# Optimization experiments

Measured on AMD Instinct MI355X. Metric: run time of the kernel, lower is better.

The kernel has to match this reference:

```python
import jax, jax.numpy as jnp
import numpy as np

L, E, D = 4, 512, 256   # layers, model dim (=2*D bidirectional), per-direction hidden
T, B = 100, 1000
EPS = 1e-5

def _layernorm(x, g, b):
    m = x.mean(-1, keepdims=True)
    v = x.var(-1, keepdims=True)
    return (x - m) / jnp.sqrt(v + EPS) * g + b

def _dir_scan(U, vf, vr, bf, br):
    # U: (T, B, 4, D) pre-projected gates; SRU elementwise recurrence over time.
    def step(c, u):
        f = jax.nn.sigmoid(u[:, 1] + vf * c + bf)
        c2 = f * c + (1.0 - f) * u[:, 0]
        r = jax.nn.sigmoid(u[:, 2] + vr * c2 + br)
        h = r * c2 + (1.0 - r) * u[:, 3]   # highway with projected residual u3
        return c2, h
    c0 = jnp.zeros((U.shape[1], U.shape[-1]), U.dtype)
    _, H = jax.lax.scan(step, c0, U)
    return H

def setup_inputs() -> dict:
    key = jax.random.key(0)
    ks = jax.random.split(key, 6)
    return {
        "sentence": jax.random.normal(ks[0], (T, B, E), jnp.float32),
        "sru_W": jax.random.normal(ks[1], (L, 2, E, 4 * D), jnp.float32) / np.float32(np.sqrt(E)),
        "sru_v": jax.random.normal(ks[2], (L, 2, 2, D), jnp.float32) * 0.05,
        "sru_b": jnp.zeros((L, 2, 2, D), jnp.float32),
        "ln_g": jnp.ones((L, E), jnp.float32),
        "ln_b": jnp.zeros((L, E), jnp.float32),
        "W1": jax.random.normal(ks[3], (E, E), jnp.float32) / np.float32(np.sqrt(E)),
        "b1": jnp.zeros((E,), jnp.float32),
        "bn_g": jnp.ones((E,), jnp.float32),
        "bn_b": jnp.zeros((E,), jnp.float32),
        "bn_mean": jnp.zeros((E,), jnp.float32),
        "bn_var": jnp.ones((E,), jnp.float32),
        "W2": jax.random.normal(ks[4], (E, 4), jnp.float32) / np.float32(np.sqrt(E)),
        "b2": jnp.zeros((4,), jnp.float32),
    }

def reference(sentence, sru_W, sru_v, sru_b, ln_g, ln_b, W1, b1, bn_g, bn_b, bn_mean, bn_var, W2, b2):
    x = sentence  # (T, B, E)
    for l in range(L):
        xl = _layernorm(x, ln_g[l], ln_b[l])
        # batched projection for both directions: (2, T, B, 4, D)
        U = jnp.einsum('tbi,dik->dtbk', xl, sru_W[l]).reshape(2, T, B, 4, D)
        Hf = _dir_scan(U[0], sru_v[l, 0, 0], sru_v[l, 0, 1], sru_b[l, 0, 0], sru_b[l, 0, 1])
        Hb = _dir_scan(U[1][::-1], sru_v[l, 1, 0], sru_v[l, 1, 1], sru_b[l, 1, 0], sru_b[l, 1, 1])[::-1]
        x = jnp.concatenate([Hf, Hb], axis=-1)  # (T, B, E)
    # head on flattened tokens (eval mode: dropout off, BN uses running stats)
    h = x.reshape(-1, E) @ W1 + b1
    h = (h - bn_mean) / jnp.sqrt(bn_var + EPS) * bn_g + bn_b
    h = jax.nn.relu(h)
    logits = h @ W2 + b2  # (T*B, 4)
    return jax.nn.log_softmax(logits, axis=-1)
```

## Files before the change

kernel.cpp:

```cpp
#include <hip/hip_runtime.h>
#include <stdint.h>

#define T_DIM 100
#define B_DIM 1000
#define E_DIM 512
#define D_DIM 256
#define L_DIM 4
#define M_TOK (T_DIM * B_DIM)
#define M_PAD 100096
#define K_DIM 512

typedef unsigned short u16;
typedef __bf16 bf16x8 __attribute__((ext_vector_type(8)));
typedef float f32x4 __attribute__((ext_vector_type(4)));
typedef unsigned short ushort8 __attribute__((ext_vector_type(8)));

__device__ __forceinline__ u16 f2bf(float f) {
  unsigned int u = __builtin_bit_cast(unsigned int, f);
  u += 0x7fffu + ((u >> 16) & 1u);
  return (u16)(u >> 16);
}
__device__ __forceinline__ float bf2f(u16 h) {
  unsigned int u = ((unsigned int)h) << 16;
  return __builtin_bit_cast(float, u);
}

__device__ __forceinline__ void gld16(const u16* g, u16* l) {
  __builtin_amdgcn_global_load_lds(
      (const __attribute__((address_space(1))) unsigned int*)g,
      (__attribute__((address_space(3))) unsigned int*)l, 16, 0, 0);
}

__global__ void transpose_cast(const float* __restrict__ in, u16* __restrict__ out,
                               int R, int C) {
  __shared__ float t[32][33];
  const int s = blockIdx.z;
  const float* ib = in + (size_t)s * R * C;
  u16* ob = out + (size_t)s * R * C;
  const int c0 = blockIdx.x * 32, r0 = blockIdx.y * 32;
  const int tx = threadIdx.x, ty = threadIdx.y;
#pragma unroll
  for (int j = 0; j < 4; ++j)
    t[ty + j * 8][tx] = ib[(size_t)(r0 + ty + j * 8) * C + c0 + tx];
  __syncthreads();
#pragma unroll
  for (int j = 0; j < 4; ++j)
    ob[(size_t)(c0 + ty + j * 8) * R + r0 + tx] = f2bf(t[tx][ty + j * 8]);
}

__global__ __launch_bounds__(256) void zero_pad(u16* __restrict__ xl) {
  const int i = blockIdx.x * 256 + threadIdx.x;
  ushort8 z = {0, 0, 0, 0, 0, 0, 0, 0};
  *(ushort8*)(xl + (size_t)M_TOK * 512 + (size_t)i * 8) = z;
}

template <typename TI>
__global__ __launch_bounds__(256) void ln_cast_kernel(
    const TI* __restrict__ x, const float* __restrict__ g,
    const float* __restrict__ b, u16* __restrict__ out) {
  const int wid = threadIdx.x >> 6, lane = threadIdx.x & 63;
  const int row = blockIdx.x * 4 + wid;
  float xe[8];
  if constexpr (sizeof(TI) == 4) {
    const float* xr = (const float*)x + (size_t)row * E_DIM + lane * 8;
    const float4 a = *(const float4*)xr;
    const float4 c = *(const float4*)(xr + 4);
    xe[0] = a.x; xe[1] = a.y; xe[2] = a.z; xe[3] = a.w;
    xe[4] = c.x; xe[5] = c.y; xe[6] = c.z; xe[7] = c.w;
  } else {
    const u16* xr = (const u16*)x + (size_t)row * E_DIM + lane * 8;
    const ushort8 hv = *(const ushort8*)xr;
#pragma unroll
    for (int u = 0; u < 8; ++u) xe[u] = bf2f(hv[u]);
  }
  float s = 0.f, q = 0.f;
#pragma unroll
  for (int u = 0; u < 8; ++u) { s += xe[u]; q += xe[u] * xe[u]; }
#pragma unroll
  for (int off = 32; off; off >>= 1) {
    s += __shfl_xor(s, off, 64);
    q += __shfl_xor(q, off, 64);
  }
  const float mean = s * (1.0f / 512.0f);
  const float var = q * (1.0f / 512.0f) - mean * mean;
  const float rstd = rsqrtf(var + 1e-5f);
  const float4 g0 = *(const float4*)(g + lane * 8);
  const float4 g1 = *(const float4*)(g + lane * 8 + 4);
  const float4 b0 = *(const float4*)(b + lane * 8);
  const float4 b1v = *(const float4*)(b + lane * 8 + 4);
  float ge[8] = {g0.x, g0.y, g0.z, g0.w, g1.x, g1.y, g1.z, g1.w};
  float be[8] = {b0.x, b0.y, b0.z, b0.w, b1v.x, b1v.y, b1v.z, b1v.w};
  ushort8 o;
#pragma unroll
  for (int u = 0; u < 8; ++u)
    o[u] = f2bf((xe[u] - mean) * rstd * ge[u] + be[u]);
  *(ushort8*)(out + (size_t)row * E_DIM + lane * 8) = o;
}

__global__ __launch_bounds__(256, 4) void gemm_bf16(
    const u16* __restrict__ A, const u16* __restrict__ B, u16* __restrict__ C,
    int N, int ntil_shift) {
  __shared__ u16 As[128 * 32];
  __shared__ u16 Bs[128 * 32];
  const int tid = threadIdx.x;
  const int wave = tid >> 6, lane = tid & 63;
  const int wm = wave >> 1, wn = wave & 1;
  const int nz = blockIdx.x;
  const int z = nz >> ntil_shift;
  const int n0 = (nz & ((1 << ntil_shift) - 1)) << 7;
  const size_t m0 = (size_t)blockIdx.y * 128;

  const int c_ld = (lane & 3) ^ ((lane >> 3) & 3);
  const u16* Ag = A + (m0 + wave * 32 + (lane >> 2)) * K_DIM + c_ld * 8;
  const u16* Bg = B + ((size_t)z * N + n0 + wave * 32 + (lane >> 2)) * K_DIM +
                  c_ld * 8;
  u16* Al = As + wave * 1024;
  u16* Bl = Bs + wave * 1024;

  f32x4 acc[4][4] = {};
  const int rA = lane & 15;
  const int ch = lane >> 4;
  const int sw = (ch ^ ((rA >> 1) & 3)) * 8;

  for (int kt = 0; kt < K_DIM; kt += 32) {
    gld16(Ag + kt, Al);
    gld16(Ag + kt + 16 * K_DIM, Al + 512);
    gld16(Bg + kt, Bl);
    gld16(Bg + kt + 16 * K_DIM, Bl + 512);
    __syncthreads();

    bf16x8 af[4], bfr[4];
#pragma unroll
    for (int mi = 0; mi < 4; ++mi)
      af[mi] = *(const bf16x8*)&As[(wm * 64 + mi * 16 + rA) * 32 + sw];
#pragma unroll
    for (int ni = 0; ni < 4; ++ni)
      bfr[ni] = *(const bf16x8*)&Bs[(wn * 64 + ni * 16 + rA) * 32 + sw];
#pragma unroll
    for (int mi = 0; mi < 4; ++mi)
#pragma unroll
      for (int ni = 0; ni < 4; ++ni)
        acc[mi][ni] = __builtin_amdgcn_mfma_f32_16x16x32_bf16(
            af[mi], bfr[ni], acc[mi][ni], 0, 0, 0);
    __syncthreads();
  }

  u16* Cb = C + (size_t)z * M_PAD * N;
  const int rr = (lane >> 4) * 4;
  const int cc = lane & 15;
#pragma unroll
  for (int mi = 0; mi < 4; ++mi) {
#pragma unroll
    for (int ni = 0; ni < 4; ++ni) {
      const size_t row = m0 + wm * 64 + mi * 16 + rr;
      const int col = n0 + wn * 64 + ni * 16 + cc;
#pragma unroll
      for (int r = 0; r < 4; ++r)
        Cb[(row + r) * N + col] = f2bf(acc[mi][ni][r]);
    }
  }
}

__global__ __launch_bounds__(256) void sru_scan(const u16* __restrict__ U,
                                                const float* __restrict__ v,
                                                const float* __restrict__ bb,
                                                u16* __restrict__ xout) {
  const int d = threadIdx.x;
  const int b = blockIdx.x;
  const int dir = blockIdx.y;
  const float vf = v[(dir * 2 + 0) * 256 + d];
  const float vr = v[(dir * 2 + 1) * 256 + d];
  const float bf = bb[(dir * 2 + 0) * 256 + d];
  const float br = bb[(dir * 2 + 1) * 256 + d];
  const u16* Ud = U + (size_t)dir * M_PAD * 1024;
  float c = 0.f;
  for (int s = 0; s < T_DIM; ++s) {
    const int t = dir ? (T_DIM - 1 - s) : s;
    const size_t base = ((size_t)t * B_DIM + b) * 1024 + d;
    const float u0 = bf2f(Ud[base]);
    const float u1 = bf2f(Ud[base + 256]);
    const float u2 = bf2f(Ud[base + 512]);
    const float u3 = bf2f(Ud[base + 768]);
    const float f = 1.f / (1.f + __expf(-(u1 + vf * c + bf)));
    c = f * c + (1.f - f) * u0;
    const float r = 1.f / (1.f + __expf(-(u2 + vr * c + br)));
    const float h = r * c + (1.f - r) * u3;
    xout[((size_t)t * B_DIM + b) * 512 + dir * 256 + d] = f2bf(h);
  }
}

__global__ __launch_bounds__(256) void head_kernel(
    const u16* __restrict__ h, const float* __restrict__ b1,
    const float* __restrict__ bn_g, const float* __restrict__ bn_b,
    const float* __restrict__ bn_mean, const float* __restrict__ bn_var,
    const float* __restrict__ W2, const float* __restrict__ b2,
    float* __restrict__ out) {
  const int wid = threadIdx.x >> 6, lane = threadIdx.x & 63;
  const int row = blockIdx.x * 4 + wid;
  const u16* hr = h + (size_t)row * E_DIM + lane * 8;
  const ushort8 hv = *(const ushort8*)hr;
  float s0 = 0.f, s1 = 0.f, s2 = 0.f, s3 = 0.f;
  const int j0 = lane * 8;
#pragma unroll
  for (int u = 0; u < 8; ++u) {
    const int j = j0 + u;
    const float hb = bf2f(hv[u]) + b1[j];
    float hn = (hb - bn_mean[j]) * rsqrtf(bn_var[j] + 1e-5f) * bn_g[j] + bn_b[j];
    hn = fmaxf(hn, 0.f);
    const float4 w = *(const float4*)(W2 + j * 4);
    s0 += hn * w.x; s1 += hn * w.y; s2 += hn * w.z; s3 += hn * w.w;
  }
#pragma unroll
  for (int off = 32; off; off >>= 1) {
    s0 += __shfl_xor(s0, off, 64);
    s1 += __shfl_xor(s1, off, 64);
    s2 += __shfl_xor(s2, off, 64);
    s3 += __shfl_xor(s3, off, 64);
  }
  if (lane == 0) {
    const float4 bv = *(const float4*)b2;
    const float l0 = s0 + bv.x, l1 = s1 + bv.y, l2 = s2 + bv.z, l3 = s3 + bv.w;
    const float mx = fmaxf(fmaxf(l0, l1), fmaxf(l2, l3));
    const float lse =
        mx + logf(__expf(l0 - mx) + __expf(l1 - mx) + __expf(l2 - mx) + __expf(l3 - mx));
    float4 o = {l0 - lse, l1 - lse, l2 - lse, l3 - lse};
    *(float4*)(out + (size_t)row * 4) = o;
  }
}

extern "C" void kernel_launch(void* const* d_in, const int* in_sizes, int n_in,
                              void* d_out, int out_size, void* d_ws, size_t ws_size,
                              hipStream_t stream) {
  const float* sentence = (const float*)d_in[0];
  const float* sru_W = (const float*)d_in[1];
  const float* sru_v = (const float*)d_in[2];
  const float* sru_b = (const float*)d_in[3];
  const float* ln_g = (const float*)d_in[4];
  const float* ln_b = (const float*)d_in[5];
  const float* W1 = (const float*)d_in[6];
  const float* b1 = (const float*)d_in[7];
  const float* bn_g = (const float*)d_in[8];
  const float* bn_b = (const float*)d_in[9];
  const float* bn_mean = (const float*)d_in[10];
  const float* bn_var = (const float*)d_in[11];
  const float* W2 = (const float*)d_in[12];
  const float* b2 = (const float*)d_in[13];

  char* ws = (char*)d_ws;
  const size_t XL_OFF = 0;
  const size_t X_OFF = XL_OFF + (size_t)M_PAD * 512 * 2;
  const size_t U_OFF = X_OFF + (size_t)M_TOK * 512 * 2;
  const size_t WT_OFF = U_OFF + (size_t)2 * M_PAD * 1024 * 2;
  const size_t W1T_OFF = WT_OFF + (size_t)8 * 512 * 1024 * 2;
  u16* xl = (u16*)(ws + XL_OFF);
  u16* x_buf = (u16*)(ws + X_OFF);
  u16* U = (u16*)(ws + U_OFF);
  u16* WT = (u16*)(ws + WT_OFF);
  u16* W1T = (u16*)(ws + W1T_OFF);
  u16* hbuf = U;

  transpose_cast<<<dim3(32, 16, 8), dim3(32, 8), 0, stream>>>(sru_W, WT, 512, 1024);
  transpose_cast<<<dim3(16, 16, 1), dim3(32, 8), 0, stream>>>(W1, W1T, 512, 512);
  zero_pad<<<24, 256, 0, stream>>>(xl);

  for (int l = 0; l < L_DIM; ++l) {
    if (l == 0)
      ln_cast_kernel<float><<<M_TOK / 4, 256, 0, stream>>>(
          sentence, ln_g, ln_b, xl);
    else
      ln_cast_kernel<u16><<<M_TOK / 4, 256, 0, stream>>>(
          x_buf, ln_g + l * 512, ln_b + l * 512, xl);
    gemm_bf16<<<dim3(16, M_PAD / 128), 256, 0, stream>>>(
        xl, WT + (size_t)l * 2 * 1024 * 512, U, 1024, 3);
    u16* xo = (l == L_DIM - 1) ? xl : x_buf;
    sru_scan<<<dim3(1000, 2), 256, 0, stream>>>(U, sru_v + l * 1024,
                                                sru_b + l * 1024, xo);
  }
  gemm_bf16<<<dim3(4, M_PAD / 128), 256, 0, stream>>>(xl, W1T, hbuf, 512, 2);
  head_kernel<<<M_TOK / 4, 256, 0, stream>>>(hbuf, b1, bn_g, bn_b, bn_mean,
                                             bn_var, W2, b2, (float*)d_out);
}
```

Baseline: 2.220 ms.

## Fuse SRU scan with next-layer LayerNorm, interleave gate columns, XCD-aware GEMM tiling

The weight transpose permutes output columns so the four SRU gates for each hidden unit sit next to each other. The scan can then fetch all four with one 8-byte load, prefetched two timesteps ahead. For layers 0-2, a new per-batch-element kernel runs both directions, keeps the full 100x512 hidden sequence in shared memory and applies the next layer's LayerNorm before writing. This removes the x_buf round trip and the separate LN launches. The GEMM grid is flattened with an XCD-aware block-to-tile mapping, and M is padded to a multiple of 1024. The catch is the ~100KB of LDS per scan block, which limits occupancy to one block per CU, and only 1000 blocks are available for the recurrence.

```diff
diff --git a/kernel.cpp b/kernel.cpp
--- a/kernel.cpp
+++ b/kernel.cpp
@@ -7,7 +7,7 @@
 #define D_DIM 256
 #define L_DIM 4
 #define M_TOK (T_DIM * B_DIM)
-#define M_PAD 100096
+#define M_PAD 100352
 #define K_DIM 512
 
 typedef unsigned short u16;
@@ -31,6 +31,7 @@
       (__attribute__((address_space(3))) unsigned int*)l, 16, 0, 0);
 }
 
+template <bool PERM>
 __global__ void transpose_cast(const float* __restrict__ in, u16* __restrict__ out,
                                int R, int C) {
   __shared__ float t[32][33];
@@ -44,8 +45,11 @@
     t[ty + j * 8][tx] = ib[(size_t)(r0 + ty + j * 8) * C + c0 + tx];
   __syncthreads();
 #pragma unroll
-  for (int j = 0; j < 4; ++j)
-    ob[(size_t)(c0 + ty + j * 8) * R + r0 + tx] = f2bf(t[tx][ty + j * 8]);
+  for (int j = 0; j < 4; ++j) {
+    const int c = c0 + ty + j * 8;
+    const int pc = PERM ? (((c & 255) << 2) | (c >> 8)) : c;
+    ob[(size_t)pc * R + r0 + tx] = f2bf(t[tx][ty + j * 8]);
+  }
 }
 
 __global__ __launch_bounds__(256) void zero_pad(u16* __restrict__ xl) {
@@ -54,25 +58,15 @@
   *(ushort8*)(xl + (size_t)M_TOK * 512 + (size_t)i * 8) = z;
 }
 
-template <typename TI>
 __global__ __launch_bounds__(256) void ln_cast_kernel(
-    const TI* __restrict__ x, const float* __restrict__ g,
+    const float* __restrict__ x, const float* __restrict__ g,
     const float* __restrict__ b, u16* __restrict__ out) {
   const int wid = threadIdx.x >> 6, lane = threadIdx.x & 63;
   const int row = blockIdx.x * 4 + wid;
-  float xe[8];
-  if constexpr (sizeof(TI) == 4) {
-    const float* xr = (const float*)x + (size_t)row * E_DIM + lane * 8;
-    const float4 a = *(const float4*)xr;
-    const float4 c = *(const float4*)(xr + 4);
-    xe[0] = a.x; xe[1] = a.y; xe[2] = a.z; xe[3] = a.w;
-    xe[4] = c.x; xe[5] = c.y; xe[6] = c.z; xe[7] = c.w;
-  } else {
-    const u16* xr = (const u16*)x + (size_t)row * E_DIM + lane * 8;
-    const ushort8 hv = *(const ushort8*)xr;
-#pragma unroll
-    for (int u = 0; u < 8; ++u) xe[u] = bf2f(hv[u]);
-  }
+  const float* xr = x + (size_t)row * E_DIM + lane * 8;
+  const float4 a = *(const float4*)xr;
+  const float4 c = *(const float4*)(xr + 4);
+  float xe[8] = {a.x, a.y, a.z, a.w, c.x, c.y, c.z, c.w};
   float s = 0.f, q = 0.f;
 #pragma unroll
   for (int u = 0; u < 8; ++u) { s += xe[u]; q += xe[u] * xe[u]; }
@@ -99,16 +93,23 @@
 
 __global__ __launch_bounds__(256, 4) void gemm_bf16(
     const u16* __restrict__ A, const u16* __restrict__ B, u16* __restrict__ C,
-    int N, int ntil_shift) {
+    int log2N, int ntil_shift) {
   __shared__ u16 As[128 * 32];
   __shared__ u16 Bs[128 * 32];
   const int tid = threadIdx.x;
   const int wave = tid >> 6, lane = tid & 63;
   const int wm = wave >> 1, wn = wave & 1;
-  const int nz = blockIdx.x;
-  const int z = nz >> ntil_shift;
-  const int n0 = (nz & ((1 << ntil_shift) - 1)) << 7;
-  const size_t m0 = (size_t)blockIdx.y * 128;
+
+  const int bid = blockIdx.x;
+  const int xcd = bid & 7;
+  const int j = bid >> 3;
+  const int nt = j & ((1 << ntil_shift) - 1);
+  const int mg = j >> ntil_shift;
+  const size_t m0 = (size_t)(xcd + (mg << 3)) * 128;
+  const int N = 1 << log2N;
+  const int colflat = nt << 7;
+  const int z = colflat >> log2N;
+  const int n0 = colflat & (N - 1);
 
   const int c_ld = (lane & 3) ^ ((lane >> 3) & 3);
   const u16* Ag = A + (m0 + wave * 32 + (lane >> 2)) * K_DIM + c_ld * 8;
@@ -158,6 +159,71 @@
       for (int r = 0; r < 4; ++r)
         Cb[(row + r) * N + col] = f2bf(acc[mi][ni][r]);
     }
+  }
+}
+
+__global__ __launch_bounds__(512) void sru_scan_ln(
+    const u16* __restrict__ U, const float* __restrict__ v,
+    const float* __restrict__ bb, const float* __restrict__ g,
+    const float* __restrict__ be, u16* __restrict__ xl) {
+  __shared__ u16 H[100 * 512];
+  const int b = blockIdx.x;
+  const int dir = threadIdx.x >> 8;
+  const int d = threadIdx.x & 255;
+  const float vf = v[(dir * 2 + 0) * 256 + d];
+  const float vr = v[(dir * 2 + 1) * 256 + d];
+  const float bfv = bb[(dir * 2 + 0) * 256 + d];
+  const float brv = bb[(dir * 2 + 1) * 256 + d];
+  const u16* p = U + (size_t)dir * M_PAD * 1024 +
+                 ((size_t)(dir ? (T_DIM - 1) : 0) * B_DIM + b) * 1024 + d * 4;
+  const intptr_t dstep = dir ? -(intptr_t)B_DIM * 1024 : (intptr_t)B_DIM * 1024;
+  ushort4 ua = *(const ushort4*)p;
+  ushort4 ub = *(const ushort4*)(p + dstep);
+  float c = 0.f;
+  int t = dir ? (T_DIM - 1) : 0;
+  const int tstep = dir ? -1 : 1;
+  for (int s = 0; s < T_DIM; ++s) {
+    ushort4 un = ub;
+    if (s + 2 < T_DIM) un = *(const ushort4*)(p + 2 * dstep);
+    const float u0 = bf2f(ua.x), u1 = bf2f(ua.y);
+    const float u2 = bf2f(ua.z), u3 = bf2f(ua.w);
+    const float f = 1.f / (1.f + __expf(-(u1 + vf * c + bfv)));
+    c = f * c + (1.f - f) * u0;
+    const float r = 1.f / (1.f + __expf(-(u2 + vr * c + brv)));
+    const float h = r * c + (1.f - r) * u3;
+    H[t * 512 + (dir << 8) + d] = f2bf(h);
+    ua = ub; ub = un; p += dstep; t += tstep;
+  }
+  __syncthreads();
+  const int wid = threadIdx.x >> 6, lane = threadIdx.x & 63;
+  const float4 g0 = *(const float4*)(g + lane * 8);
+  const float4 g1 = *(const float4*)(g + lane * 8 + 4);
+  const float4 b0 = *(const float4*)(be + lane * 8);
+  const float4 b1v = *(const float4*)(be + lane * 8 + 4);
+  const float ge[8] = {g0.x, g0.y, g0.z, g0.w, g1.x, g1.y, g1.z, g1.w};
+  const float bev[8] = {b0.x, b0.y, b0.z, b0.w, b1v.x, b1v.y, b1v.z, b1v.w};
+  for (int tr = wid; tr < T_DIM; tr += 8) {
+    const ushort8 hv = *(const ushort8*)&H[tr * 512 + lane * 8];
+    float xe[8];
+    float s = 0.f, q = 0.f;
+#pragma unroll
+    for (int u = 0; u < 8; ++u) {
+      xe[u] = bf2f(hv[u]);
+      s += xe[u]; q += xe[u] * xe[u];
+    }
+#pragma unroll
+    for (int off = 32; off; off >>= 1) {
+      s += __shfl_xor(s, off, 64);
+      q += __shfl_xor(q, off, 64);
+    }
+    const float mean = s * (1.0f / 512.0f);
+    const float var = q * (1.0f / 512.0f) - mean * mean;
+    const float rstd = rsqrtf(var + 1e-5f);
+    ushort8 o;
+#pragma unroll
+    for (int u = 0; u < 8; ++u)
+      o[u] = f2bf((xe[u] - mean) * rstd * ge[u] + bev[u]);
+    *(ushort8*)(xl + ((size_t)tr * B_DIM + b) * 512 + lane * 8) = o;
   }
 }
 
@@ -170,22 +236,27 @@
   const int dir = blockIdx.y;
   const float vf = v[(dir * 2 + 0) * 256 + d];
   const float vr = v[(dir * 2 + 1) * 256 + d];
-  const float bf = bb[(dir * 2 + 0) * 256 + d];
-  const float br = bb[(dir * 2 + 1) * 256 + d];
-  const u16* Ud = U + (size_t)dir * M_PAD * 1024;
+  const float bfv = bb[(dir * 2 + 0) * 256 + d];
+  const float brv = bb[(dir * 2 + 1) * 256 + d];
+  const u16* p = U + (size_t)dir * M_PAD * 1024 +
+                 ((size_t)(dir ? (T_DIM - 1) : 0) * B_DIM + b) * 1024 + d * 4;
+  const intptr_t dstep = dir ? -(intptr_t)B_DIM * 1024 : (intptr_t)B_DIM * 1024;
+  ushort4 ua = *(const ushort4*)p;
+  ushort4 ub = *(const ushort4*)(p + dstep);
   float c = 0.f;
+  int t = dir ? (T_DIM - 1) : 0;
+  const int tstep = dir ? -1 : 1;
   for (int s = 0; s < T_DIM; ++s) {
-    const int t = dir ? (T_DIM - 1 - s) : s;
-    const size_t base = ((size_t)t * B_DIM + b) * 1024 + d;
-    const float u0 = bf2f(Ud[base]);
-    const float u1 = bf2f(Ud[base + 256]);
-    const float u2 = bf2f(Ud[base + 512]);
-    const float u3 = bf2f(Ud[base + 768]);
-    const float f = 1.f / (1.f + __expf(-(u1 + vf * c + bf)));
+    ushort4 un = ub;
+    if (s + 2 < T_DIM) un = *(const ushort4*)(p + 2 * dstep);
+    const float u0 = bf2f(ua.x), u1 = bf2f(ua.y);
+    const float u2 = bf2f(ua.z), u3 = bf2f(ua.w);
+    const float f = 1.f / (1.f + __expf(-(u1 + vf * c + bfv)));
     c = f * c + (1.f - f) * u0;
-    const float r = 1.f / (1.f + __expf(-(u2 + vr * c + br)));
+    const float r = 1.f / (1.f + __expf(-(u2 + vr * c + brv)));
     const float h = r * c + (1.f - r) * u3;
-    xout[((size_t)t * B_DIM + b) * 512 + dir * 256 + d] = f2bf(h);
+    xout[((size_t)t * B_DIM + b) * 512 + (dir << 8) + d] = f2bf(h);
+    ua = ub; ub = un; p += dstep; t += tstep;
   }
 }
 
@@ -248,35 +319,33 @@
 
   char* ws = (char*)d_ws;
   const size_t XL_OFF = 0;
-  const size_t X_OFF = XL_OFF + (size_t)M_PAD * 512 * 2;
-  const size_t U_OFF = X_OFF + (size_t)M_TOK * 512 * 2;
+  const size_t U_OFF = XL_OFF + (size_t)M_PAD * 512 * 2;
   const size_t WT_OFF = U_OFF + (size_t)2 * M_PAD * 1024 * 2;
   const size_t W1T_OFF = WT_OFF + (size_t)8 * 512 * 1024 * 2;
   u16* xl = (u16*)(ws + XL_OFF);
-  u16* x_buf = (u16*)(ws + X_OFF);
   u16* U = (u16*)(ws + U_OFF);
   u16* WT = (u16*)(ws + WT_OFF);
   u16* W1T = (u16*)(ws + W1T_OFF);
   u16* hbuf = U;
 
-  transpose_cast<<<dim3(32, 16, 8), dim3(32, 8), 0, stream>>>(sru_W, WT, 512, 1024);
-  transpose_cast<<<dim3(16, 16, 1), dim3(32, 8), 0, stream>>>(W1, W1T, 512, 512);
-  zero_pad<<<24, 256, 0, stream>>>(xl);
-
+  transpose_cast<true><<<dim3(32, 16, 8), dim3(32, 8), 0, stream>>>(sru_W, WT, 512, 1024);
+  transpose_cast<false><<<dim3(16, 16, 1), dim3(32, 8), 0, stream>>>(W1, W1T, 512, 512);
+  zero_pad<<<88, 256, 0, stream>>>(xl);
+
+  ln_cast_kernel<<<M_TOK / 4, 256, 0, stream>>>(sentence, ln_g, ln_b, xl);
   for (int l = 0; l < L_DIM; ++l) {
-    if (l == 0)
-      ln_cast_kernel<float><<<M_TOK / 4, 256, 0, stream>>>(
-          sentence, ln_g, ln_b, xl);
+    gemm_bf16<<<784 * 16, 256, 0, stream>>>(
+        xl, WT + (size_t)l * 2 * 1024 * 512, U, 10, 4);
+    if (l < L_DIM - 1)
+      sru_scan_ln<<<B_DIM, 512, 0, stream>>>(U, sru_v + l * 1024,
+                                             sru_b + l * 1024,
+                                             ln_g + (l + 1) * 512,
+                                             ln_b + (l + 1) * 512, xl);
     else
-      ln_cast_kernel<u16><<<M_TOK / 4, 256, 0, stream>>>(
-          x_buf, ln_g + l * 512, ln_b + l * 512, xl);
-    gemm_bf16<<<dim3(16, M_PAD / 128), 256, 0, stream>>>(
-        xl, WT + (size_t)l * 2 * 1024 * 512, U, 1024, 3);
-    u16* xo = (l == L_DIM - 1) ? xl : x_buf;
-    sru_scan<<<dim3(1000, 2), 256, 0, stream>>>(U, sru_v + l * 1024,
-                                                sru_b + l * 1024, xo);
-  }
-  gemm_bf16<<<dim3(4, M_PAD / 128), 256, 0, stream>>>(xl, W1T, hbuf, 512, 2);
+      sru_scan<<<dim3(B_DIM, 2), 256, 0, stream>>>(U, sru_v + l * 1024,
+                                                   sru_b + l * 1024, xl);
+  }
+  gemm_bf16<<<784 * 4, 256, 0, stream>>>(xl, W1T, hbuf, 9, 2);
   head_kernel<<<M_TOK / 4, 256, 0, stream>>>(hbuf, b1, bn_g, bn_b, bn_mean,
                                              bn_var, W2, b2, (float*)d_out);
 }
```

New measurement: 2.368 ms. 1.07x slower.

## Interleave SRU gate columns, widen GEMM K-tile, and remap blocks per XCD

Applied to the files above, without the earlier changes.

The projection weights are permuted so the four gate values for each hidden unit land next to each other in U. The scan can then read them with one 8-byte load per step, and it prefetches two timesteps ahead. The GEMM now uses a 64-wide K tile with a new XOR swizzle and swaps operands so each lane writes four contiguous bf16 outputs. Blocks are remapped so consecutive M tiles go to the same XCD, and M_PAD grows to a multiple of 1024 rows to fit this mapping. Doubling LDS per block lowers the occupancy bound from 4 to 3 blocks, and the extra padding adds some wasted rows.

```diff
diff --git a/kernel.cpp b/kernel.cpp
--- a/kernel.cpp
+++ b/kernel.cpp
@@ -7,7 +7,7 @@
 #define D_DIM 256
 #define L_DIM 4
 #define M_TOK (T_DIM * B_DIM)
-#define M_PAD 100096
+#define M_PAD 100352
 #define K_DIM 512
 
 typedef unsigned short u16;
@@ -31,6 +31,7 @@
       (__attribute__((address_space(3))) unsigned int*)l, 16, 0, 0);
 }
 
+template <bool PERM>
 __global__ void transpose_cast(const float* __restrict__ in, u16* __restrict__ out,
                                int R, int C) {
   __shared__ float t[32][33];
@@ -44,8 +45,11 @@
     t[ty + j * 8][tx] = ib[(size_t)(r0 + ty + j * 8) * C + c0 + tx];
   __syncthreads();
 #pragma unroll
-  for (int j = 0; j < 4; ++j)
-    ob[(size_t)(c0 + ty + j * 8) * R + r0 + tx] = f2bf(t[tx][ty + j * 8]);
+  for (int j = 0; j < 4; ++j) {
+    const int c = c0 + ty + j * 8;
+    const int pc = PERM ? (((c & 255) << 2) | (c >> 8)) : c;
+    ob[(size_t)pc * R + r0 + tx] = f2bf(t[tx][ty + j * 8]);
+  }
 }
 
 __global__ __launch_bounds__(256) void zero_pad(u16* __restrict__ xl) {
@@ -97,66 +101,78 @@
   *(ushort8*)(out + (size_t)row * E_DIM + lane * 8) = o;
 }
 
-__global__ __launch_bounds__(256, 4) void gemm_bf16(
+__global__ __launch_bounds__(256, 3) void gemm_bf16(
     const u16* __restrict__ A, const u16* __restrict__ B, u16* __restrict__ C,
-    int N, int ntil_shift) {
-  __shared__ u16 As[128 * 32];
-  __shared__ u16 Bs[128 * 32];
+    int log2N, int ntil_shift) {
+  __shared__ u16 As[128 * 64];
+  __shared__ u16 Bs[128 * 64];
   const int tid = threadIdx.x;
   const int wave = tid >> 6, lane = tid & 63;
   const int wm = wave >> 1, wn = wave & 1;
-  const int nz = blockIdx.x;
-  const int z = nz >> ntil_shift;
-  const int n0 = (nz & ((1 << ntil_shift) - 1)) << 7;
-  const size_t m0 = (size_t)blockIdx.y * 128;
-
-  const int c_ld = (lane & 3) ^ ((lane >> 3) & 3);
-  const u16* Ag = A + (m0 + wave * 32 + (lane >> 2)) * K_DIM + c_ld * 8;
-  const u16* Bg = B + ((size_t)z * N + n0 + wave * 32 + (lane >> 2)) * K_DIM +
+
+  const int bid = blockIdx.x;
+  const int xcd = bid & 7;
+  const int j = bid >> 3;
+  const int nt = j & ((1 << ntil_shift) - 1);
+  const int mg = j >> ntil_shift;
+  const size_t m0 = (size_t)(xcd + (mg << 3)) * 128;
+  const int N = 1 << log2N;
+  const int colflat = nt << 7;
+  const int z = colflat >> log2N;
+  const int n0 = colflat & (N - 1);
+
+  const int c_ld = (lane & 7) ^ (lane >> 3);
+  const u16* Ag = A + (m0 + wave * 32 + (lane >> 3)) * K_DIM + c_ld * 8;
+  const u16* Bg = B + ((size_t)z * N + n0 + wave * 32 + (lane >> 3)) * K_DIM +
                   c_ld * 8;
-  u16* Al = As + wave * 1024;
-  u16* Bl = Bs + wave * 1024;
+  u16* Al = As + wave * 32 * 64;
+  u16* Bl = Bs + wave * 32 * 64;
 
   f32x4 acc[4][4] = {};
   const int rA = lane & 15;
-  const int ch = lane >> 4;
-  const int sw = (ch ^ ((rA >> 1) & 3)) * 8;
-
-  for (int kt = 0; kt < K_DIM; kt += 32) {
-    gld16(Ag + kt, Al);
-    gld16(Ag + kt + 16 * K_DIM, Al + 512);
-    gld16(Bg + kt, Bl);
-    gld16(Bg + kt + 16 * K_DIM, Bl + 512);
+  const int q = lane >> 4;
+
+  for (int kt = 0; kt < K_DIM; kt += 64) {
+#pragma unroll
+    for (int i = 0; i < 4; ++i) {
+      gld16(Ag + kt + (size_t)i * 8 * K_DIM, Al + i * 512);
+      gld16(Bg + kt + (size_t)i * 8 * K_DIM, Bl + i * 512);
+    }
     __syncthreads();
 
-    bf16x8 af[4], bfr[4];
-#pragma unroll
-    for (int mi = 0; mi < 4; ++mi)
-      af[mi] = *(const bf16x8*)&As[(wm * 64 + mi * 16 + rA) * 32 + sw];
-#pragma unroll
-    for (int ni = 0; ni < 4; ++ni)
-      bfr[ni] = *(const bf16x8*)&Bs[(wn * 64 + ni * 16 + rA) * 32 + sw];
-#pragma unroll
-    for (int mi = 0; mi < 4; ++mi)
+#pragma unroll
+    for (int kk = 0; kk < 2; ++kk) {
+      const int st = ((kk * 4 + q) ^ (rA & 7)) * 8;
+      bf16x8 af[4], bfr[4];
+#pragma unroll
+      for (int mi = 0; mi < 4; ++mi)
+        af[mi] = *(const bf16x8*)&As[(wm * 64 + mi * 16 + rA) * 64 + st];
 #pragma unroll
       for (int ni = 0; ni < 4; ++ni)
-        acc[mi][ni] = __builtin_amdgcn_mfma_f32_16x16x32_bf16(
-            af[mi], bfr[ni], acc[mi][ni], 0, 0, 0);
+        bfr[ni] = *(const bf16x8*)&Bs[(wn * 64 + ni * 16 + rA) * 64 + st];
+#pragma unroll
+      for (int mi = 0; mi < 4; ++mi)
+#pragma unroll
+        for (int ni = 0; ni < 4; ++ni)
+          acc[mi][ni] = __builtin_amdgcn_mfma_f32_16x16x32_bf16(
+              bfr[ni], af[mi], acc[mi][ni], 0, 0, 0);
+    }
     __syncthreads();
   }
 
   u16* Cb = C + (size_t)z * M_PAD * N;
-  const int rr = (lane >> 4) * 4;
-  const int cc = lane & 15;
 #pragma unroll
   for (int mi = 0; mi < 4; ++mi) {
+    const size_t token = m0 + wm * 64 + mi * 16 + rA;
 #pragma unroll
     for (int ni = 0; ni < 4; ++ni) {
-      const size_t row = m0 + wm * 64 + mi * 16 + rr;
-      const int col = n0 + wn * 64 + ni * 16 + cc;
-#pragma unroll
-      for (int r = 0; r < 4; ++r)
-        Cb[(row + r) * N + col] = f2bf(acc[mi][ni][r]);
+      const int ncol = n0 + wn * 64 + ni * 16 + q * 4;
+      ushort4 o;
+      o.x = f2bf(acc[mi][ni][0]);
+      o.y = f2bf(acc[mi][ni][1]);
+      o.z = f2bf(acc[mi][ni][2]);
+      o.w = f2bf(acc[mi][ni][3]);
+      *(ushort4*)&Cb[token * N + ncol] = o;
     }
   }
 }
@@ -170,22 +186,27 @@
   const int dir = blockIdx.y;
   const float vf = v[(dir * 2 + 0) * 256 + d];
   const float vr = v[(dir * 2 + 1) * 256 + d];
-  const float bf = bb[(dir * 2 + 0) * 256 + d];
-  const float br = bb[(dir * 2 + 1) * 256 + d];
-  const u16* Ud = U + (size_t)dir * M_PAD * 1024;
+  const float bfv = bb[(dir * 2 + 0) * 256 + d];
+  const float brv = bb[(dir * 2 + 1) * 256 + d];
+  const u16* p = U + (size_t)dir * M_PAD * 1024 +
+                 ((size_t)(dir ? (T_DIM - 1) : 0) * B_DIM + b) * 1024 + d * 4;
+  const intptr_t dstep = dir ? -(intptr_t)B_DIM * 1024 : (intptr_t)B_DIM * 1024;
+  ushort4 ua = *(const ushort4*)p;
+  ushort4 ub = *(const ushort4*)(p + dstep);
   float c = 0.f;
+  int t = dir ? (T_DIM - 1) : 0;
+  const int tstep = dir ? -1 : 1;
   for (int s = 0; s < T_DIM; ++s) {
-    const int t = dir ? (T_DIM - 1 - s) : s;
-    const size_t base = ((size_t)t * B_DIM + b) * 1024 + d;
-    const float u0 = bf2f(Ud[base]);
-    const float u1 = bf2f(Ud[base + 256]);
-    const float u2 = bf2f(Ud[base + 512]);
-    const float u3 = bf2f(Ud[base + 768]);
-    const float f = 1.f / (1.f + __expf(-(u1 + vf * c + bf)));
+    ushort4 un = ub;
+    if (s + 2 < T_DIM) un = *(const ushort4*)(p + 2 * dstep);
+    const float u0 = bf2f(ua.x), u1 = bf2f(ua.y);
+    const float u2 = bf2f(ua.z), u3 = bf2f(ua.w);
+    const float f = 1.f / (1.f + __expf(-(u1 + vf * c + bfv)));
     c = f * c + (1.f - f) * u0;
-    const float r = 1.f / (1.f + __expf(-(u2 + vr * c + br)));
+    const float r = 1.f / (1.f + __expf(-(u2 + vr * c + brv)));
     const float h = r * c + (1.f - r) * u3;
-    xout[((size_t)t * B_DIM + b) * 512 + dir * 256 + d] = f2bf(h);
+    xout[((size_t)t * B_DIM + b) * 512 + (dir << 8) + d] = f2bf(h);
+    ua = ub; ub = un; p += dstep; t += tstep;
   }
 }
 
@@ -248,20 +269,20 @@
 
   char* ws = (char*)d_ws;
   const size_t XL_OFF = 0;
-  const size_t X_OFF = XL_OFF + (size_t)M_PAD * 512 * 2;
-  const size_t U_OFF = X_OFF + (size_t)M_TOK * 512 * 2;
+  const size_t XB_OFF = XL_OFF + (size_t)M_PAD * 512 * 2;
+  const size_t U_OFF = XB_OFF + (size_t)M_TOK * 512 * 2;
   const size_t WT_OFF = U_OFF + (size_t)2 * M_PAD * 1024 * 2;
   const size_t W1T_OFF = WT_OFF + (size_t)8 * 512 * 1024 * 2;
   u16* xl = (u16*)(ws + XL_OFF);
-  u16* x_buf = (u16*)(ws + X_OFF);
+  u16* x_buf = (u16*)(ws + XB_OFF);
   u16* U = (u16*)(ws + U_OFF);
   u16* WT = (u16*)(ws + WT_OFF);
   u16* W1T = (u16*)(ws + W1T_OFF);
   u16* hbuf = U;
 
-  transpose_cast<<<dim3(32, 16, 8), dim3(32, 8), 0, stream>>>(sru_W, WT, 512, 1024);
-  transpose_cast<<<dim3(16, 16, 1), dim3(32, 8), 0, stream>>>(W1, W1T, 512, 512);
-  zero_pad<<<24, 256, 0, stream>>>(xl);
+  transpose_cast<true><<<dim3(32, 16, 8), dim3(32, 8), 0, stream>>>(sru_W, WT, 512, 1024);
+  transpose_cast<false><<<dim3(16, 16, 1), dim3(32, 8), 0, stream>>>(W1, W1T, 512, 512);
+  zero_pad<<<88, 256, 0, stream>>>(xl);
 
   for (int l = 0; l < L_DIM; ++l) {
     if (l == 0)
@@ -270,13 +291,13 @@
     else
       ln_cast_kernel<u16><<<M_TOK / 4, 256, 0, stream>>>(
           x_buf, ln_g + l * 512, ln_b + l * 512, xl);
-    gemm_bf16<<<dim3(16, M_PAD / 128), 256, 0, stream>>>(
-        xl, WT + (size_t)l * 2 * 1024 * 512, U, 1024, 3);
+    gemm_bf16<<<784 * 16, 256, 0, stream>>>(
+        xl, WT + (size_t)l * 2 * 1024 * 512, U, 10, 4);
     u16* xo = (l == L_DIM - 1) ? xl : x_buf;
-    sru_scan<<<dim3(1000, 2), 256, 0, stream>>>(U, sru_v + l * 1024,
-                                                sru_b + l * 1024, xo);
-  }
-  gemm_bf16<<<dim3(4, M_PAD / 128), 256, 0, stream>>>(xl, W1T, hbuf, 512, 2);
+    sru_scan<<<dim3(B_DIM, 2), 256, 0, stream>>>(U, sru_v + l * 1024,
+                                                 sru_b + l * 1024, xo);
+  }
+  gemm_bf16<<<784 * 4, 256, 0, stream>>>(xl, W1T, hbuf, 9, 2);
   head_kernel<<<M_TOK / 4, 256, 0, stream>>>(hbuf, b1, bn_g, bn_b, bn_mean,
                                              bn_var, W2, b2, (float*)d_out);
 }
```

Result: no change. 2.242 ms (+1.0%).
